# Kernel optimization log

Hardware: AMD Instinct MI355X
Metric: run time of the kernel (lower is better)

## Reference

```python
import jax, jax.numpy as jnp
import numpy as np

B, S, HID = 1, 8192, 768
H, D = 12, 64          # num heads, head dim (HID = H*D)
W = 256                # one-sided attention window


def _shift_chunks(xc, C):
    # xc: [B, C, w, H, D] -> prev/next chunk copies padded with zeros
    prev = jnp.pad(xc, ((0, 0), (1, 0), (0, 0), (0, 0), (0, 0)))[:, :C]
    nxt = jnp.pad(xc, ((0, 0), (0, 1), (0, 0), (0, 0), (0, 0)))[:, 1:]
    return jnp.concatenate([prev, xc, nxt], axis=2)  # [B, C, 3w, H, D]


def sliding_window_attention(q, k, v, w):
    # q,k,v: [B, S, H, D]; q already scaled. Band width 2w+1.
    b, s, h, d = q.shape
    c = s // w
    qc = q.reshape(b, c, w, h, d)
    k3 = _shift_chunks(k.reshape(b, c, w, h, d), c)  # [b,c,3w,h,d]
    v3 = _shift_chunks(v.reshape(b, c, w, h, d), c)
    # scores of each query chunk against its 3-chunk key neighborhood
    scores3 = jnp.einsum('bcxhd,bcyhd->bhcxy', qc, k3)  # [b,h,c,w,3w]
    rows = jnp.arange(w)
    offs = jnp.arange(2 * w + 1)
    gidx = rows[:, None] + offs[None, :]  # [w, 2w+1] local key index p+j
    band = scores3[..., rows[:, None], gidx]  # [b,h,c,w,2w+1]
    # mask keys outside [0, S) (same effect as mask_invalid_locations)
    gq = jnp.arange(s).reshape(c, w)                    # global query pos
    keypos = gq[..., None] + (offs - w)                 # [c,w,2w+1]
    valid = (keypos >= 0) & (keypos < s)
    band = jnp.where(valid[None, None], band, -jnp.inf)
    prob = jax.nn.softmax(band, axis=-1)
    prob = jnp.where(valid[None, None], prob, 0.0)
    # scatter band probs back to 3w layout, then banded PV matmul
    prob3 = jnp.zeros(band.shape[:-1] + (3 * w,), band.dtype)
    prob3 = prob3.at[..., rows[:, None], gidx].set(prob)  # [b,h,c,w,3w]
    ctx = jnp.einsum('bhcxy,bcyhd->bcxhd', prob3, v3)
    return ctx.reshape(b, s, h, d)


def setup_inputs() -> dict:
    key = jax.random.key(0)
    ks = jax.random.split(key, 4)
    sc = 1.0 / np.sqrt(HID)
    return {
        'hidden_states': jax.random.normal(ks[0], (B, S, HID), jnp.float32),
        'Wq': jax.random.normal(ks[1], (HID, HID), jnp.float32) * sc,
        'bq': jnp.zeros((HID,), jnp.float32),
        'Wk': jax.random.normal(ks[2], (HID, HID), jnp.float32) * sc,
        'bk': jnp.zeros((HID,), jnp.float32),
        'Wv': jax.random.normal(ks[3], (HID, HID), jnp.float32) * sc,
        'bv': jnp.zeros((HID,), jnp.float32),
    }


def reference(hidden_states, Wq, bq, Wk, bk, Wv, bv):
    b, s, hid = hidden_states.shape
    q = (hidden_states @ Wq + bq).reshape(b, s, H, D)
    k = (hidden_states @ Wk + bk).reshape(b, s, H, D)
    v = (hidden_states @ Wv + bv).reshape(b, s, H, D)
    q = q / jnp.asarray(np.sqrt(D), q.dtype)
    ctx = sliding_window_attention(q, k, v, W)  # [b,s,H,D]
    return ctx.reshape(b, s, hid)
```

## Files before the change

kernel.cpp:

```cpp
#include <hip/hip_runtime.h>
#include <hip/hip_bf16.h>

#define S_LEN 8192
#define HID 768
#define NH 12
#define HD 64
#define WIN 256

typedef __bf16 bf16x8 __attribute__((ext_vector_type(8)));
typedef float f32x4 __attribute__((ext_vector_type(4)));
using bf16_t = __hip_bfloat16;

#define MFMA(a, b, c) __builtin_amdgcn_mfma_f32_16x16x32_bf16(a, b, c, 0, 0, 0)

__device__ __forceinline__ void gl2lds16(const bf16_t* g, bf16_t* l) {
  __builtin_amdgcn_global_load_lds(
      (const __attribute__((address_space(1))) void*)g,
      (__attribute__((address_space(3))) void*)l, 16, 0, 0);
}

__global__ __launch_bounds__(256) void prep(const float* __restrict__ hs,
                                            bf16_t* __restrict__ hb,
                                            const float* __restrict__ Wq,
                                            const float* __restrict__ Wk,
                                            const float* __restrict__ Wv,
                                            bf16_t* __restrict__ Wt) {
  int bx = blockIdx.x;
  int tid = threadIdx.x;
  if (bx < 6144) {
    int i = (bx * 256 + tid) * 4;
    float4 v = *reinterpret_cast<const float4*>(hs + i);
    union { ushort4 u; bf16_t b[4]; } H;
    H.b[0] = __float2bfloat16(v.x);
    H.b[1] = __float2bfloat16(v.y);
    H.b[2] = __float2bfloat16(v.z);
    H.b[3] = __float2bfloat16(v.w);
    *reinterpret_cast<ushort4*>(hb + i) = H.u;
    return;
  }
  __shared__ float t[32][33];
  int b = bx - 6144;
  int z = b / 576;
  int r = b % 576;
  int n0 = (r / 24) * 32, k0 = (r % 24) * 32;
  const float* src = (z == 0) ? Wq : ((z == 1) ? Wk : Wv);
  int tx = tid & 31, ty = tid >> 5;
  for (int i = 0; i < 4; ++i)
    t[ty + i * 8][tx] = src[(k0 + ty + i * 8) * HID + n0 + tx];
  __syncthreads();
  bf16_t* dst = Wt + z * HID * HID;
  for (int i = 0; i < 4; ++i)
    dst[(n0 + ty + i * 8) * HID + k0 + tx] = __float2bfloat16(t[tx][ty + i * 8]);
}

__global__ __launch_bounds__(256, 3) void qkv_gemm(
    const bf16_t* __restrict__ hb, const bf16_t* __restrict__ Wt,
    const float* __restrict__ bq, const float* __restrict__ bk,
    const float* __restrict__ bv,
    bf16_t* __restrict__ Qw, bf16_t* __restrict__ Kw, bf16_t* __restrict__ Vt) {
  __shared__ __align__(16) bf16_t sA[2][64 * 64];
  __shared__ __align__(16) bf16_t sB[2][128 * 64];
  int bl = blockIdx.y * 128 + blockIdx.x;
  int xcd = bl & 7;
  int j = bl >> 3;
  int m0 = (xcd * 16 + (j & 15)) * 64;
  int rest = j >> 4;
  int zq = rest / 6;
  int nn0 = (rest % 6) * 128;
  int n0g = zq * HID + nn0;
  int tid = threadIdx.x;
  int w = tid >> 6, lane = tid & 63, lm = lane & 15, qd = lane >> 4;
  int wm = w & 1, wn = w >> 1;

  int srow = w * 8 + (lane >> 3);
  int sc8 = (lane & 7) ^ ((lane >> 3) & 7);
  const bf16_t* gA = hb + (m0 + srow) * HID + sc8 * 8;
  const bf16_t* gB = Wt + (n0g + srow) * HID + sc8 * 8;
  int sx0 = lm & 7;

#define QSTAGE(kk, bb)                                                       \
  {                                                                          \
    _Pragma("unroll") for (int u = 0; u < 2; ++u)                            \
        gl2lds16(gA + (u * 32) * HID + (kk), sA[bb] + u * 2048 + w * 512);   \
    _Pragma("unroll") for (int u = 0; u < 4; ++u)                            \
        gl2lds16(gB + (u * 32) * HID + (kk), sB[bb] + u * 2048 + w * 512);   \
  }

  QSTAGE(0, 0);
  __syncthreads();

  f32x4 acc[8] = {};
  for (int kt = 0; kt < 12; ++kt) {
    int b = kt & 1;
    if (kt < 11) QSTAGE((kt + 1) * 64, b ^ 1);
#pragma unroll
    for (int half = 0; half < 2; ++half) {
      int ca = (qd + 4 * half) ^ sx0;
      bf16x8 fa[2], fb[4];
#pragma unroll
      for (int i = 0; i < 2; ++i)
        fa[i] = *reinterpret_cast<const bf16x8*>(
            sA[b] + (wm * 32 + i * 16 + lm) * 64 + ca * 8);
#pragma unroll
      for (int i = 0; i < 4; ++i)
        fb[i] = *reinterpret_cast<const bf16x8*>(
            sB[b] + (wn * 64 + i * 16 + lm) * 64 + ca * 8);
      if (zq == 2) {
#pragma unroll
        for (int j2 = 0; j2 < 4; ++j2)
#pragma unroll
          for (int i = 0; i < 2; ++i)
            acc[j2 * 2 + i] = MFMA(fb[j2], fa[i], acc[j2 * 2 + i]);
      } else {
#pragma unroll
        for (int i = 0; i < 2; ++i)
#pragma unroll
          for (int j2 = 0; j2 < 4; ++j2)
            acc[i * 4 + j2] = MFMA(fa[i], fb[j2], acc[i * 4 + j2]);
      }
    }
    __syncthreads();
  }

  if (zq != 2) {
    const float* bias = zq ? bk : bq;
    bf16_t* dst = zq ? Kw : Qw;
    float scale = zq ? 1.0f : 0.125f;
#pragma unroll
    for (int j2 = 0; j2 < 4; ++j2) {
      int nl = nn0 + wn * 64 + j2 * 16 + lm;
      float bb = bias[nl];
      int h = nl >> 6, d = nl & 63;
#pragma unroll
      for (int i = 0; i < 2; ++i)
#pragma unroll
        for (int r = 0; r < 4; ++r) {
          int m = m0 + wm * 32 + i * 16 + qd * 4 + r;
          dst[(h * S_LEN + m) * HD + d] =
              __float2bfloat16((acc[i * 4 + j2][r] + bb) * scale);
        }
    }
  } else {
#pragma unroll
    for (int j2 = 0; j2 < 4; ++j2)
#pragma unroll
      for (int r = 0; r < 4; ++r) {
        int nl = nn0 + wn * 64 + j2 * 16 + qd * 4 + r;
        float bb = bv[nl];
#pragma unroll
        for (int i = 0; i < 2; ++i) {
          int m = m0 + wm * 32 + i * 16 + lm;
          Vt[nl * S_LEN + m] = __float2bfloat16(acc[j2 * 2 + i][r] + bb);
        }
      }
  }
}

__global__ __launch_bounds__(256, 3) void swa_kernel(
    const bf16_t* __restrict__ Qw, const bf16_t* __restrict__ Kw,
    const bf16_t* __restrict__ Vt, float* __restrict__ out) {
  __shared__ __align__(16) bf16_t sK[2][64 * 64];
  __shared__ __align__(16) bf16_t sV[2][64 * 64];
  __shared__ __align__(16) bf16_t sP[4 * 32 * 64];
  int h = blockIdx.y;
  int nb = blockIdx.x;
  int q0 = (((nb & 7) << 3) | (nb >> 3)) * 128;
  int tid = threadIdx.x;
  int w = tid >> 6, lane = tid & 63, lm = lane & 15, qd = lane >> 4;
  int xb = q0 + w * 32;

  int qoff = (h * S_LEN + xb + lm) * HD + qd * 8;
  bf16x8 aq00 = *reinterpret_cast<const bf16x8*>(Qw + qoff);
  bf16x8 aq01 = *reinterpret_cast<const bf16x8*>(Qw + qoff + 32);
  bf16x8 aq10 = *reinterpret_cast<const bf16x8*>(Qw + qoff + 16 * HD);
  bf16x8 aq11 = *reinterpret_cast<const bf16x8*>(Qw + qoff + 16 * HD + 32);

  f32x4 o0[4] = {}, o1[4] = {};
  float lsum0 = 0.f, lsum1 = 0.f;

  int y_begin = q0 - WIN; if (y_begin < 0) y_begin = 0;
  int y_end = q0 + 128 + WIN; if (y_end > S_LEN) y_end = S_LEN;
  int ntiles = (y_end - y_begin) >> 6;
  const bf16_t* Kh = Kw + h * S_LEN * HD;
  const bf16_t* Vh = Vt + h * HD * S_LEN;
  bf16_t* sPw = sP + w * 32 * 64;

  int srow = w * 8 + (lane >> 3);
  int sc8 = (lane & 7) ^ ((lane >> 3) & 7);
  int sx0 = lm & 7;

#define STAGE(y0, b)                                                    \
  {                                                                     \
    const bf16_t* kg = Kh + ((y0) + srow) * HD + sc8 * 8;               \
    gl2lds16(kg, &sK[b][w * 512]);                                      \
    gl2lds16(kg + 32 * HD, &sK[b][2048 + w * 512]);                     \
    const bf16_t* vg = Vh + srow * S_LEN + (y0) + sc8 * 8;              \
    gl2lds16(vg, &sV[b][w * 512]);                                      \
    gl2lds16(vg + 32 * S_LEN, &sV[b][2048 + w * 512]);                  \
  }

  STAGE(y_begin, 0);
  __syncthreads();

  for (int t = 0; t < ntiles; ++t) {
    int y0 = y_begin + t * 64;
    if (t + 1 < ntiles) STAGE(y0 + 64, (t + 1) & 1);
    int b = t & 1;
    f32x4 s0[4] = {}, s1[4] = {};
#pragma unroll
    for (int nt = 0; nt < 4; ++nt) {
      const bf16_t* kr = &sK[b][(nt * 16 + lm) * 64];
      bf16x8 b0 = *reinterpret_cast<const bf16x8*>(kr + (qd ^ sx0) * 8);
      bf16x8 b1 = *reinterpret_cast<const bf16x8*>(kr + ((qd + 4) ^ sx0) * 8);
      s0[nt] = MFMA(b0, aq00, s0[nt]);
      s0[nt] = MFMA(b1, aq01, s0[nt]);
      s1[nt] = MFMA(b0, aq10, s1[nt]);
      s1[nt] = MFMA(b1, aq11, s1[nt]);
    }
    int dyw = y0 - xb;
    bool edge = (dyw > 193) || (dyw < -225);
#pragma unroll
    for (int g = 0; g < 2; ++g) {
      const f32x4* sg = g ? s1 : s0;
      float lacc = 0.f;
#pragma unroll
      for (int nt = 0; nt < 4; ++nt) {
        union { ushort4 u; bf16_t b[4]; } P;
#pragma unroll
        for (int r = 0; r < 4; ++r) {
          float pv;
          if (edge) {
            int dlt = (y0 + nt * 16 + qd * 4 + r) - (xb + g * 16 + lm);
            pv = (dlt <= WIN && dlt >= -WIN) ? __expf(sg[nt][r]) : 0.f;
          } else {
            pv = __expf(sg[nt][r]);
          }
          lacc += pv;
          P.b[r] = __float2bfloat16(pv);
        }
        *reinterpret_cast<ushort4*>(
            sPw + (g * 16 + lm) * 64 +
            (((2 * nt + (qd >> 1)) ^ sx0) * 8) + (qd & 1) * 4) = P.u;
      }
      if (g) lsum1 += lacc; else lsum0 += lacc;
    }
    bf16x8 ap00 =
        *reinterpret_cast<const bf16x8*>(sPw + lm * 64 + ((qd ^ sx0) * 8));
    bf16x8 ap01 = *reinterpret_cast<const bf16x8*>(sPw + lm * 64 +
                                                   (((qd + 4) ^ sx0) * 8));
    bf16x8 ap10 = *reinterpret_cast<const bf16x8*>(sPw + (16 + lm) * 64 +
                                                   ((qd ^ sx0) * 8));
    bf16x8 ap11 = *reinterpret_cast<const bf16x8*>(sPw + (16 + lm) * 64 +
                                                   (((qd + 4) ^ sx0) * 8));
#pragma unroll
    for (int nt = 0; nt < 4; ++nt) {
      const bf16_t* vr = &sV[b][(nt * 16 + lm) * 64];
      bf16x8 v0 = *reinterpret_cast<const bf16x8*>(vr + (qd ^ sx0) * 8);
      bf16x8 v1 = *reinterpret_cast<const bf16x8*>(vr + ((qd + 4) ^ sx0) * 8);
      o0[nt] = MFMA(ap00, v0, o0[nt]);
      o0[nt] = MFMA(ap01, v1, o0[nt]);
      o1[nt] = MFMA(ap10, v0, o1[nt]);
      o1[nt] = MFMA(ap11, v1, o1[nt]);
    }
    __syncthreads();
  }
  lsum0 += __shfl_xor(lsum0, 16);
  lsum0 += __shfl_xor(lsum0, 32);
  lsum1 += __shfl_xor(lsum1, 16);
  lsum1 += __shfl_xor(lsum1, 32);
#pragma unroll
  for (int r = 0; r < 4; ++r) {
    float inv0 = 1.f / __shfl(lsum0, qd * 4 + r);
    int x0 = xb + qd * 4 + r;
#pragma unroll
    for (int nt = 0; nt < 4; ++nt)
      out[x0 * HID + h * HD + nt * 16 + lm] = o0[nt][r] * inv0;
    float inv1 = 1.f / __shfl(lsum1, qd * 4 + r);
    int x1 = xb + 16 + qd * 4 + r;
#pragma unroll
    for (int nt = 0; nt < 4; ++nt)
      out[x1 * HID + h * HD + nt * 16 + lm] = o1[nt][r] * inv1;
  }
}

extern "C" void kernel_launch(void* const* d_in, const int* in_sizes, int n_in,
                              void* d_out, int out_size, void* d_ws, size_t ws_size,
                              hipStream_t stream) {
  const float* hs = (const float*)d_in[0];
  const float* Wq = (const float*)d_in[1];
  const float* bq = (const float*)d_in[2];
  const float* Wk = (const float*)d_in[3];
  const float* bk = (const float*)d_in[4];
  const float* Wv = (const float*)d_in[5];
  const float* bv = (const float*)d_in[6];
  float* out = (float*)d_out;

  const int NSH = S_LEN * HID;
  const int NW = 3 * HID * HID;
  bf16_t* p = (bf16_t*)d_ws;
  bf16_t* hb = p; p += NSH;
  bf16_t* Wt = p; p += NW;
  bf16_t* Qw = p; p += NSH;
  bf16_t* Kw = p; p += NSH;
  bf16_t* Vt = p; p += NSH;

  prep<<<dim3(6144 + 1728), dim3(256), 0, stream>>>(hs, hb, Wq, Wk, Wv, Wt);
  qkv_gemm<<<dim3(128, 18), dim3(256), 0, stream>>>(
      hb, Wt, bq, bk, bv, Qw, Kw, Vt);
  swa_kernel<<<dim3(64, 12), dim3(256), 0, stream>>>(Qw, Kw, Vt, out);
}
```

Baseline: 157.7 us.

## Load K/V fragments directly from global memory instead of LDS staging

Removes the double-buffered LDS staging of K and V tiles and the per-tile block barrier; each wave now reads its MFMA operands for K and V directly from global memory. The occupancy hint is raised from 3 to 4 blocks per CU, using the freed LDS. This avoids barrier synchronization and LDS traffic, but each wave redundantly fetches the same K/V tiles and loses the asynchronous prefetch overlap, relying on caches and occupancy to hide latency.

```diff
diff --git a/kernel.cpp b/kernel.cpp
--- a/kernel.cpp
+++ b/kernel.cpp
@@ -156,11 +156,9 @@
   }
 }
 
-__global__ __launch_bounds__(256, 3) void swa_kernel(
+__global__ __launch_bounds__(256, 4) void swa_kernel(
     const bf16_t* __restrict__ Qw, const bf16_t* __restrict__ Kw,
     const bf16_t* __restrict__ Vt, float* __restrict__ out) {
-  __shared__ __align__(16) bf16_t sK[2][64 * 64];
-  __shared__ __align__(16) bf16_t sV[2][64 * 64];
   __shared__ __align__(16) bf16_t sP[4 * 32 * 64];
   int h = blockIdx.y;
   int nb = blockIdx.x;
@@ -184,34 +182,16 @@
   const bf16_t* Kh = Kw + h * S_LEN * HD;
   const bf16_t* Vh = Vt + h * HD * S_LEN;
   bf16_t* sPw = sP + w * 32 * 64;
-
-  int srow = w * 8 + (lane >> 3);
-  int sc8 = (lane & 7) ^ ((lane >> 3) & 7);
   int sx0 = lm & 7;
-
-#define STAGE(y0, b)                                                    \
-  {                                                                     \
-    const bf16_t* kg = Kh + ((y0) + srow) * HD + sc8 * 8;               \
-    gl2lds16(kg, &sK[b][w * 512]);                                      \
-    gl2lds16(kg + 32 * HD, &sK[b][2048 + w * 512]);                     \
-    const bf16_t* vg = Vh + srow * S_LEN + (y0) + sc8 * 8;              \
-    gl2lds16(vg, &sV[b][w * 512]);                                      \
-    gl2lds16(vg + 32 * S_LEN, &sV[b][2048 + w * 512]);                  \
-  }
-
-  STAGE(y_begin, 0);
-  __syncthreads();
 
   for (int t = 0; t < ntiles; ++t) {
     int y0 = y_begin + t * 64;
-    if (t + 1 < ntiles) STAGE(y0 + 64, (t + 1) & 1);
-    int b = t & 1;
     f32x4 s0[4] = {}, s1[4] = {};
 #pragma unroll
     for (int nt = 0; nt < 4; ++nt) {
-      const bf16_t* kr = &sK[b][(nt * 16 + lm) * 64];
-      bf16x8 b0 = *reinterpret_cast<const bf16x8*>(kr + (qd ^ sx0) * 8);
-      bf16x8 b1 = *reinterpret_cast<const bf16x8*>(kr + ((qd + 4) ^ sx0) * 8);
+      const bf16_t* kr = Kh + (size_t)(y0 + nt * 16 + lm) * HD + qd * 8;
+      bf16x8 b0 = *reinterpret_cast<const bf16x8*>(kr);
+      bf16x8 b1 = *reinterpret_cast<const bf16x8*>(kr + 32);
       s0[nt] = MFMA(b0, aq00, s0[nt]);
       s0[nt] = MFMA(b1, aq01, s0[nt]);
       s1[nt] = MFMA(b0, aq10, s1[nt]);
@@ -254,15 +234,14 @@
                                                    (((qd + 4) ^ sx0) * 8));
 #pragma unroll
     for (int nt = 0; nt < 4; ++nt) {
-      const bf16_t* vr = &sV[b][(nt * 16 + lm) * 64];
-      bf16x8 v0 = *reinterpret_cast<const bf16x8*>(vr + (qd ^ sx0) * 8);
-      bf16x8 v1 = *reinterpret_cast<const bf16x8*>(vr + ((qd + 4) ^ sx0) * 8);
+      const bf16_t* vr = Vh + (size_t)(nt * 16 + lm) * S_LEN + y0 + qd * 8;
+      bf16x8 v0 = *reinterpret_cast<const bf16x8*>(vr);
+      bf16x8 v1 = *reinterpret_cast<const bf16x8*>(vr + 32);
       o0[nt] = MFMA(ap00, v0, o0[nt]);
       o0[nt] = MFMA(ap01, v1, o0[nt]);
       o1[nt] = MFMA(ap10, v0, o1[nt]);
       o1[nt] = MFMA(ap11, v1, o1[nt]);
     }
-    __syncthreads();
   }
   lsum0 += __shfl_xor(lsum0, 16);
   lsum0 += __shfl_xor(lsum0, 32);
```

Result: slower. 184.6 us (+17.0%).
